# Kernel optimization log

Measured on AMD Instinct MI355X. Metric: run time of the kernel, lower is better.

## Reference

```python
import jax, jax.numpy as jnp
import numpy as np

N_MOL, E_MOL = 50000, 200000
N_PRO, E_PRO = 100000, 800000


def segment_softmax(e, seg, n):
    # e: [E, H] logits, softmax over edges grouped by target node `seg`
    m = jax.ops.segment_max(e, seg, num_segments=n)
    m = jnp.where(jnp.isfinite(m), m, jnp.zeros_like(m))
    ex = jnp.exp(e - m[seg])
    s = jax.ops.segment_sum(ex, seg, num_segments=n)
    return ex / (s[seg] + 1e-16)


def gat_conv(x, edge_index, W, a_src, a_dst, b, heads, out_ch):
    # torch_geometric GATConv (concat=True, add_self_loops=True, neg slope 0.2, eval mode)
    n = x.shape[0]
    loop = jnp.arange(n, dtype=edge_index.dtype)
    src = jnp.concatenate([edge_index[0], loop])
    dst = jnp.concatenate([edge_index[1], loop])
    h = (x @ W).reshape(n, heads, out_ch)            # [N,H,C]
    alpha_s = jnp.sum(h * a_src, axis=-1)            # [N,H]
    alpha_d = jnp.sum(h * a_dst, axis=-1)            # [N,H]
    e = jax.nn.leaky_relu(alpha_s[src] + alpha_d[dst], 0.2)  # [E,H]
    alpha = segment_softmax(e, dst, n)               # [E,H]
    out = jax.ops.segment_sum(alpha[:, :, None] * h[src], dst, num_segments=n)  # [N,H,C]
    return out.reshape(n, heads * out_ch) + b


def gcn_conv(x, edge_index, edge_weight, W, b):
    # torch_geometric GCNConv with edge_weight (add_self_loops=True, sym norm)
    n = x.shape[0]
    loop = jnp.arange(n, dtype=edge_index.dtype)
    src = jnp.concatenate([edge_index[0], loop])
    dst = jnp.concatenate([edge_index[1], loop])
    w = jnp.concatenate([edge_weight, jnp.ones((n,), x.dtype)])
    deg = jax.ops.segment_sum(w, dst, num_segments=n)
    dinv = jnp.where(deg > 0, deg ** -0.5, jnp.zeros_like(deg))
    norm = dinv[src] * w * dinv[dst]                 # [E]
    h = x @ W                                        # [N,C]
    return jax.ops.segment_sum(norm[:, None] * h[src], dst, num_segments=n) + b


def setup_inputs() -> dict:
    key = jax.random.key(0)
    ks = iter(jax.random.split(key, 32))
    rn = lambda shape, s=0.1: jax.random.normal(next(ks), shape, dtype=jnp.float32) * s
    inp = {
        "mol_x": rn((N_MOL, 78), 1.0),
        "mol_edge_index": jax.random.randint(next(ks), (2, E_MOL), 0, N_MOL, dtype=jnp.int32),
        "pro_x": rn((N_PRO, 33), 1.0),
        "pro_edge_index": jax.random.randint(next(ks), (2, E_PRO), 0, N_PRO, dtype=jnp.int32),
        "pro_edge_weight": jax.random.uniform(next(ks), (E_PRO,), dtype=jnp.float32),
        # mol_conv1: GAT 78->78, heads=2
        "W1": rn((78, 156)), "a_src1": rn((2, 78)), "a_dst1": rn((2, 78)), "b1": jnp.zeros((156,), jnp.float32),
        # mol_conv2: GAT 156->156, heads=2
        "W2": rn((156, 312)), "a_src2": rn((2, 156)), "a_dst2": rn((2, 156)), "b2": jnp.zeros((312,), jnp.float32),
        # mol_conv3: GAT 312->312, heads=1
        "W3": rn((312, 312)), "a_src3": rn((1, 312)), "a_dst3": rn((1, 312)), "b3": jnp.zeros((312,), jnp.float32),
        # pro_conv1: GCN 33->33
        "Wp1": rn((33, 33)), "bp1": jnp.zeros((33,), jnp.float32),
        # pro_conv2: GAT 33->66, heads=2
        "Wp2": rn((33, 132)), "ap_src2": rn((2, 66)), "ap_dst2": rn((2, 66)), "bp2": jnp.zeros((132,), jnp.float32),
        # pro_conv3: GAT 132->132, heads=1
        "Wp3": rn((132, 132)), "ap_src3": rn((1, 132)), "ap_dst3": rn((1, 132)), "bp3": jnp.zeros((132,), jnp.float32),
    }
    return inp


def reference(mol_x, mol_edge_index, pro_x, pro_edge_index, pro_edge_weight,
              W1, a_src1, a_dst1, b1, W2, a_src2, a_dst2, b2, W3, a_src3, a_dst3, b3,
              Wp1, bp1, Wp2, ap_src2, ap_dst2, bp2, Wp3, ap_src3, ap_dst3, bp3):
    # mol branch (per CPI_GAT.forward): conv1 -> relu -> conv2 -> relu -> conv3
    x = jax.nn.relu(gat_conv(mol_x, mol_edge_index, W1, a_src1, a_dst1, b1, 2, 78))
    x = jax.nn.relu(gat_conv(x, mol_edge_index, W2, a_src2, a_dst2, b2, 2, 156))
    x = gat_conv(x, mol_edge_index, W3, a_src3, a_dst3, b3, 1, 312)
    # pro branch: gcn -> relu -> gat -> relu -> gat -> relu
    xt = jax.nn.relu(gcn_conv(pro_x, pro_edge_index, pro_edge_weight, Wp1, bp1))
    xt = jax.nn.relu(gat_conv(xt, pro_edge_index, Wp2, ap_src2, ap_dst2, bp2, 2, 66))
    xt = jax.nn.relu(gat_conv(xt, pro_edge_index, Wp3, ap_src3, ap_dst3, bp3, 1, 132))
    return (x, xt)
```

## Files before the change

### kernel.cpp

```cpp
#include <hip/hip_runtime.h>
#include <cstdint>
#include <cstddef>

#define WAVE 64
#define NPB 4

#define TBM 128
#define TBN 128
#define TBK 32
#define LDK 40

typedef short s16x8 __attribute__((ext_vector_type(8)));
typedef float f32x4 __attribute__((ext_vector_type(4)));

__device__ __forceinline__ unsigned short f2bf(float f) {
    unsigned int u = __float_as_uint(f);
    unsigned int r = (u + 0x7fffu + ((u >> 16) & 1u)) >> 16;
    return (unsigned short)r;
}
__device__ __forceinline__ float bf2f_lo(unsigned int v) { return __uint_as_float(v << 16); }
__device__ __forceinline__ float bf2f_hi(unsigned int v) { return __uint_as_float(v & 0xffff0000u); }
__device__ __forceinline__ float lrelu02(float e) { return (e > 0.f) ? e : 0.2f * e; }


// ... 64 lines not shown
    }

#pragma unroll
    for (int mt = 0; mt < 4; mt++) {
#pragma unroll
        for (int r = 0; r < 4; r++) {
            int row = rowBase + wm + mt * 16 + quad * 4 + r;
            if (row < N) {
#pragma unroll
                for (int nt = 0; nt < 4; nt++) {
                    int col = colBase + wn + nt * 16 + l15;
                    float v = acc[mt][nt][r];
                    if (col < M) {
                        float v2 = v;
                        if (bias != nullptr) {
                            v2 += bias[col];
                            if (relu) v2 = fmaxf(v2, 0.f);
                        }
                        Cbf[(size_t)row * Mp + col] = f2bf(v2);
                    } else if (col < zpadTo) {
                        Cbf[(size_t)row * Mp + col] = 0;
                    } else if (asb != nullptr && col < M + 2 * H) {
                        int t = col - M;
                        if (t < H) asb[(size_t)row * H + t] = v;
                        else adb[(size_t)row * H + (t - H)] = v;
                    }
                }
            }
        }
    }
}


template <int SLOTS, int G, int H, bool SM, int SWEEPS, bool GCN, bool NEXTA>
__device__ __forceinline__ void agg_body(const unsigned short* __restrict__ hfeat,
                                         const float* __restrict__ as_, const float* __restrict__ ad_,
                                         const float* __restrict__ dinv,
                                         const int* __restrict__ rowp, const int2* __restrict__ cpack,
                                         const float* __restrict__ bias,
                                         float* __restrict__ out_f, unsigned short* __restrict__ out_bf,
                                         const float* __restrict__ vanf, int vald,
                                         float* __restrict__ asn, float* __restrict__ adn_o,
                                         int HC, int ldo, int relu, int n, int lane) {
    constexpr int ROWB = SWEEPS * SLOTS * 16;
    int g = lane / SLOTS;
    int slot = lane - g * SLOTS;
    bool act = (g < G);
    int C = HC / H;
    int beg = rowp[n], end = rowp[n + 1];

    float adn[H], msub[H];
    float di = 0.f;
    if (GCN) {
        di = dinv[n];
    } else {
#pragma unroll
        for (int h = 0; h < H; h++) {
            adn[h] = ad_[(size_t)n * H + h];
            msub[h] = lrelu02(as_[(size_t)n * H + h] + adn[h]);
        }
    }

    int ch0[SWEEPS];
    bool h1q[SWEEPS][4];
#pragma unroll
    for (int sw = 0; sw < SWEEPS; sw++) {
        ch0[sw] = (sw * SLOTS + slot) * 8;
#pragma unroll
        for (int q = 0; q < 4; q++) h1q[sw][q] = (H == 2) && ((ch0[sw] + 2 * q) >= C);
    }

    float sfw = GCN ? di * di : 1.f;
    float accx[SWEEPS][4], accy[SWEEPS][4];
#pragma unroll
    for (int sw = 0; sw < SWEEPS; sw++)
#pragma unroll
        for (int q = 0; q < 4; q++) { accx[sw][q] = 0.f; accy[sw][q] = 0.f; }
    if (act && g == 0) {
#pragma unroll
        for (int sw = 0; sw < SWEEPS; sw++) {
            uint4 v = *(const uint4*)((const char*)hfeat + (size_t)n * ROWB + (sw * SLOTS + slot) * 16);
            unsigned int vv[4] = {v.x, v.y, v.z, v.w};
#pragma unroll
            for (int q = 0; q < 4; q++) { accx[sw][q] = sfw * bf2f_lo(vv[q]); accy[sw][q] = sfw * bf2f_hi(vv[q]); }
        }
    }

    float wsum[H];
#pragma unroll
    for (int h = 0; h < H; h++) wsum[h] = 0.f;

    for (int base = beg; base < end; base += WAVE) {
        int cnt = end - base;
        if (cnt > WAVE) cnt = WAVE;
        int s_l = 0;
        float w_l[H];
#pragma unroll
        for (int h = 0; h < H; h++) w_l[h] = 0.f;
        if (lane < cnt) {
            int2 pk = cpack[base + lane];
            s_l = pk.x;
            if (GCN) {
                w_l[0] = dinv[s_l] * __int_as_float(pk.y) * di;
            } else {
#pragma unroll
                for (int h = 0; h < H; h++)
                    w_l[h] = __expf(lrelu02(as_[(size_t)s_l * H + h] + adn[h]) - msub[h]);
            }
            if (SM) {
#pragma unroll
                for (int h = 0; h < H; h++) wsum[h] += w_l[h];
            }
        }
        for (int j0 = 0; j0 < cnt; j0 += 2 * G) {
            int sA;
            float wA[H];
            uint4 vA[SWEEPS];
            {
                int jj = j0 + g;
                bool pad = (jj >= cnt);
                if (jj > cnt - 1) jj = cnt - 1;
                int ba = jj << 2;
                sA = __builtin_amdgcn_ds_bpermute(ba, s_l);
#pragma unroll
                for (int h = 0; h < H; h++) {
                    float t = __uint_as_float(
                        (unsigned)__builtin_amdgcn_ds_bpermute(ba, (int)__float_as_uint(w_l[h])));
                    wA[h] = pad ? 0.f : t;
                }
                if (act) {
#pragma unroll
                    for (int sw = 0; sw < SWEEPS; sw++) {
                        unsigned voff = (unsigned)sA * ROWB + (sw * SLOTS + slot) * 16;
                        vA[sw] = *(const uint4*)((const char*)hfeat + voff);
                    }
                }
            }
            bool haveB = (j0 + G < cnt);
            int sB;
            float wB[H];
            uint4 vB[SWEEPS];
            if (haveB) {
                int jj = j0 + G + g;
                bool pad = (jj >= cnt);
                if (jj > cnt - 1) jj = cnt - 1;
                int ba = jj << 2;
                sB = __builtin_amdgcn_ds_bpermute(ba, s_l);
#pragma unroll
                for (int h = 0; h < H; h++) {
                    float t = __uint_as_float(
                        (unsigned)__builtin_amdgcn_ds_bpermute(ba, (int)__float_as_uint(w_l[h])));
                    wB[h] = pad ? 0.f : t;
                }
                if (act) {
#pragma unroll
                    for (int sw = 0; sw < SWEEPS; sw++) {
                        unsigned voff = (unsigned)sB * ROWB + (sw * SLOTS + slot) * 16;
                        vB[sw] = *(const uint4*)((const char*)hfeat + voff);
                    }
                }
            }
            if (act) {
#pragma unroll
                for (int sw = 0; sw < SWEEPS; sw++) {
                    unsigned int va[4] = {vA[sw].x, vA[sw].y, vA[sw].z, vA[sw].w};
#pragma unroll
                    for (int q = 0; q < 4; q++) {
                        float wq = (H == 2) ? (h1q[sw][q] ? wA[1] : wA[0]) : wA[0];
                        accx[sw][q] += wq * bf2f_lo(va[q]);
                        accy[sw][q] += wq * bf2f_hi(va[q]);
                    }
                }
                if (haveB) {
#pragma unroll
                    for (int sw = 0; sw < SWEEPS; sw++) {
                        unsigned int ub[4] = {vB[sw].x, vB[sw].y, vB[sw].z, vB[sw].w};
#pragma unroll
                        for (int q = 0; q < 4; q++) {
                            float wq = (H == 2) ? (h1q[sw][q] ? wB[1] : wB[0]) : wB[0];
                            accx[sw][q] += wq * bf2f_lo(ub[q]);
                            accy[sw][q] += wq * bf2f_hi(ub[q]);
                        }
                    }
                }
            }
        }
    }

    if (G == 3) {
#pragma unroll
        for (int sw = 0; sw < SWEEPS; sw++)
#pragma unroll
            for (int q = 0; q < 4; q++) {
                int b1a = (lane + SLOTS) << 2, b2a = (lane + 2 * SLOTS) << 2;
                float t1 = __uint_as_float((unsigned)__builtin_amdgcn_ds_bpermute(b1a, (int)__float_as_uint(accx[sw][q])));
                float t2 = __uint_as_float((unsigned)__builtin_amdgcn_ds_bpermute(b2a, (int)__float_as_uint(accx[sw][q])));
                accx[sw][q] += t1 + t2;
                float t3 = __uint_as_float((unsigned)__builtin_amdgcn_ds_bpermute(b1a, (int)__float_as_uint(accy[sw][q])));
                float t4 = __uint_as_float((unsigned)__builtin_amdgcn_ds_bpermute(b2a, (int)__float_as_uint(accy[sw][q])));
                accy[sw][q] += t3 + t4;
            }
    } else if (G == 8) {
#pragma unroll
        for (int st = 4; st >= 1; st >>= 1) {
            int ba = (lane + st * SLOTS) << 2;
#pragma unroll
            for (int sw = 0; sw < SWEEPS; sw++)
#pragma unroll
                for (int q = 0; q < 4; q++) {
                    accx[sw][q] += __uint_as_float((unsigned)__builtin_amdgcn_ds_bpermute(ba, (int)__float_as_uint(accx[sw][q])));
                    accy[sw][q] += __uint_as_float((unsigned)__builtin_amdgcn_ds_bpermute(ba, (int)__float_as_uint(accy[sw][q])));
                }
        }
    }

    float rs[H];
    if (SM) {
#pragma unroll
        for (int h = 0; h < H; h++) {
            float t = wsum[h];
            for (int off = 32; off > 0; off >>= 1) t += __shfl_xor(t, off);
            rs[h] = 1.f / (1.f + t + 1e-16f);
        }
    } else {
#pragma unroll
        for (int h = 0; h < H; h++) rs[h] = 1.f;
    }

    float ps[4] = {0.f, 0.f, 0.f, 0.f};
    if (lane < SLOTS) {
#pragma unroll
        for (int sw = 0; sw < SWEEPS; sw++) {
            float o[8];
#pragma unroll
            for (int q = 0; q < 4; q++) {
                float r = (H == 2) ? (h1q[sw][q] ? rs[1] : rs[0]) : rs[0];
                int c0 = ch0[sw] + 2 * q;
                float b0 = (c0 < HC) ? bias[c0] : 0.f;
                float b1v = (c0 + 1 < HC) ? bias[c0 + 1] : 0.f;
                float o0 = accx[sw][q] * r + b0;
                float o1 = accy[sw][q] * r + b1v;
                if (relu) { o0 = fmaxf(o0, 0.f); o1 = fmaxf(o1, 0.f); }
                if (c0 >= HC) o0 = 0.f;
                if (c0 + 1 >= HC) o1 = 0.f;
                o[2 * q] = o0;
                o[2 * q + 1] = o1;
            }
            if (NEXTA) {
#pragma unroll
                for (int j = 0; j < 8; j++) {
                    int c = ch0[sw] + j;
#pragma unroll
                    for (int th = 0; th < 4; th++) ps[th] += o[j] * vanf[th * vald + c];
                }
            }
            if (out_bf) {
                uint4 pk;
                unsigned* pp = (unsigned*)&pk;
#pragma unroll
                for (int q = 0; q < 4; q++)
                    pp[q] = (unsigned)f2bf(o[2 * q]) | ((unsigned)f2bf(o[2 * q + 1]) << 16);
                *(uint4*)((char*)out_bf + (size_t)n * ((size_t)ldo * 2) + (sw * SLOTS + slot) * 16) = pk;
            } else {
#pragma unroll
                for (int half = 0; half < 2; half++) {
                    int c0 = ch0[sw] + half * 4;
                    if (c0 < HC) {
                        float4 f4 = make_float4(o[half * 4], o[half * 4 + 1], o[half * 4 + 2], o[half * 4 + 3]);
                        *(float4*)(out_f + (size_t)n * HC + c0) = f4;
                    }
                }
            }
        }
    }
    if (NEXTA) {
#pragma unroll
        for (int th = 0; th < 4; th++)
            for (int off = 32; off > 0; off >>= 1) ps[th] += __shfl_xor(ps[th], off);
        if (lane == 0) {
            asn[(size_t)n * 2 + 0] = ps[0];
            asn[(size_t)n * 2 + 1] = ps[1];
            adn_o[(size_t)n * 2 + 0] = ps[2];
            adn_o[(size_t)n * 2 + 1] = ps[3];
        }
    }
}


template <int SLOTS, int G>
__device__ __forceinline__ void aggN_body(const unsigned short* __restrict__ x,
                                          const float* __restrict__ as_, const float* __restrict__ ad_,
                                          const int* __restrict__ rowp, const int2* __restrict__ cpack,
                                          unsigned short* __restrict__ A2, int n, int lane) {
    constexpr int ROWB = SLOTS * 16;
    int g = lane / SLOTS;
    int slot = lane - g * SLOTS;
    bool act = (g < G);
    int beg = rowp[n], end = rowp[n + 1];

    float adn[2], msub[2];
#pragma unroll
    for (int h = 0; h < 2; h++) {
        adn[h] = ad_[(size_t)n * 2 + h];
        msub[h] = lrelu02(as_[(size_t)n * 2 + h] + adn[h]);
    }

    float ax[2][4], ay[2][4];
#pragma unroll
    for (int h = 0; h < 2; h++)
#pragma unroll
        for (int q = 0; q < 4; q++) { ax[h][q] = 0.f; ay[h][q] = 0.f; }
    if (act && g == 0) {
        uint4 v = *(const uint4*)((const char*)x + (size_t)n * ROWB + slot * 16);
        unsigned int vv[4] = {v.x, v.y, v.z, v.w};
#pragma unroll
        for (int q = 0; q < 4; q++) {
            float lo = bf2f_lo(vv[q]), hi = bf2f_hi(vv[q]);
            ax[0][q] = lo; ax[1][q] = lo;
            ay[0][q] = hi; ay[1][q] = hi;
        }
    }

    float wsum[2] = {0.f, 0.f};

    for (int base = beg; base < end; base += WAVE) {
        int cnt = end - base;
        if (cnt > WAVE) cnt = WAVE;
        int s_l = 0;
        float w_l[2] = {0.f, 0.f};
        if (lane < cnt) {
            s_l = cpack[base + lane].x;
#pragma unroll
            for (int h = 0; h < 2; h++)
                w_l[h] = __expf(lrelu02(as_[(size_t)s_l * 2 + h] + adn[h]) - msub[h]);
            wsum[0] += w_l[0];
            wsum[1] += w_l[1];
        }
        for (int j0 = 0; j0 < cnt; j0 += 2 * G) {
            int sA;
            float wA[2];
            uint4 vA;
            {
                int jj = j0 + g;
                bool pad = (jj >= cnt);
                if (jj > cnt - 1) jj = cnt - 1;
                int ba = jj << 2;
                sA = __builtin_amdgcn_ds_bpermute(ba, s_l);
#pragma unroll
                for (int h = 0; h < 2; h++) {
                    float t = __uint_as_float(
                        (unsigned)__builtin_amdgcn_ds_bpermute(ba, (int)__float_as_uint(w_l[h])));
                    wA[h] = pad ? 0.f : t;
                }
                if (act) vA = *(const uint4*)((const char*)x + (unsigned)sA * ROWB + slot * 16);
            }
            bool haveB = (j0 + G < cnt);
            int sB;
            float wB[2];
            uint4 vB;
            if (haveB) {
                int jj = j0 + G + g;
                bool pad = (jj >= cnt);
                if (jj > cnt - 1) jj = cnt - 1;
                int ba = jj << 2;
                sB = __builtin_amdgcn_ds_bpermute(ba, s_l);
#pragma unroll
                for (int h = 0; h < 2; h++) {
                    float t = __uint_as_float(
                        (unsigned)__builtin_amdgcn_ds_bpermute(ba, (int)__float_as_uint(w_l[h])));
                    wB[h] = pad ? 0.f : t;
                }
                if (act) vB = *(const uint4*)((const char*)x + (unsigned)sB * ROWB + slot * 16);
            }
            if (act) {
                unsigned int va[4] = {vA.x, vA.y, vA.z, vA.w};
#pragma unroll
                for (int q = 0; q < 4; q++) {
                    float lo = bf2f_lo(va[q]), hi = bf2f_hi(va[q]);
                    ax[0][q] += wA[0] * lo; ax[1][q] += wA[1] * lo;
                    ay[0][q] += wA[0] * hi; ay[1][q] += wA[1] * hi;
                }
                if (haveB) {
                    unsigned int ub[4] = {vB.x, vB.y, vB.z, vB.w};
#pragma unroll
                    for (int q = 0; q < 4; q++) {
                        float lo = bf2f_lo(ub[q]), hi = bf2f_hi(ub[q]);
                        ax[0][q] += wB[0] * lo; ax[1][q] += wB[1] * lo;
                        ay[0][q] += wB[0] * hi; ay[1][q] += wB[1] * hi;
                    }
                }
            }
        }
    }

    if (G == 3) {
#pragma unroll
        for (int h = 0; h < 2; h++)
#pragma unroll
            for (int q = 0; q < 4; q++) {
                int b1a = (lane + SLOTS) << 2, b2a = (lane + 2 * SLOTS) << 2;
                float t1 = __uint_as_float((unsigned)__builtin_amdgcn_ds_bpermute(b1a, (int)__float_as_uint(ax[h][q])));
                float t2 = __uint_as_float((unsigned)__builtin_amdgcn_ds_bpermute(b2a, (int)__float_as_uint(ax[h][q])));
                ax[h][q] += t1 + t2;
                float t3 = __uint_as_float((unsigned)__builtin_amdgcn_ds_bpermute(b1a, (int)__float_as_uint(ay[h][q])));
                float t4 = __uint_as_float((unsigned)__builtin_amdgcn_ds_bpermute(b2a, (int)__float_as_uint(ay[h][q])));
                ay[h][q] += t3 + t4;
            }
    } else if (G == 8) {
#pragma unroll
        for (int st = 4; st >= 1; st >>= 1) {
            int ba = (lane + st * SLOTS) << 2;
#pragma unroll
            for (int h = 0; h < 2; h++)
#pragma unroll
                for (int q = 0; q < 4; q++) {
                    ax[h][q] += __uint_as_float((unsigned)__builtin_amdgcn_ds_bpermute(ba, (int)__float_as_uint(ax[h][q])));
                    ay[h][q] += __uint_as_float((unsigned)__builtin_amdgcn_ds_bpermute(ba, (int)__float_as_uint(ay[h][q])));
                }
        }
    }

    float rs[2];
#pragma unroll
    for (int h = 0; h < 2; h++) {
        float t = wsum[h];
        for (int off = 32; off > 0; off >>= 1) t += __shfl_xor(t, off);
        rs[h] = 1.f / (1.f + t + 1e-16f);
    }

    if (lane < SLOTS) {
#pragma unroll
        for (int h = 0; h < 2; h++) {
            uint4 pk;
            unsigned* pp = (unsigned*)&pk;
#pragma unroll
            for (int q = 0; q < 4; q++) {
                float o0 = ax[h][q] * rs[h];
                float o1 = ay[h][q] * rs[h];
                pp[q] = (unsigned)f2bf(o0) | ((unsigned)f2bf(o1) << 16);
            }
            *(uint4*)((char*)A2 + (size_t)n * (2 * ROWB) + h * ROWB + slot * 16) = pk;
        }
    }
}


__device__ __forceinline__ void cvtw1(const float* __restrict__ W, unsigned short* __restrict__ WT,
                                      int K, int M, int Kp, int i) {
    int m = i / Kp;
    int k = i - m * Kp;
    WT[i] = (k < K) ? f2bf(W[(long long)k * M + m]) : (unsigned short)0;
}

__device__ __forceinline__ void cvtw_bd(const float* __restrict__ W, unsigned short* __restrict__ WT,
                                        int K, int M, int C, int Kp, int Kph, int i) {
    int m = i / Kp;
    int k = i - m * Kp;
    unsigned short v = 0;
    if (m < M) {
        int hm = m / C;
        int kk = k - hm * Kph;
        if (kk >= 0 && kk < K) v = f2bf(W[(long long)kk * M + m]);
    }
    WT[i] = v;
}

__device__ __forceinline__ void prep1(const float* __restrict__ W, const float* __restrict__ a_src,
                                      const float* __restrict__ a_dst, unsigned short* __restrict__ WT,
                                      int K, int M, int C, int Kp, int H, int b, int lane) {
    int k = b % Kp;
    int th = b / Kp;
    int t = th / H;
    int h = th - t * H;
    size_t orow = (size_t)(M + t * H + h) * Kp;
    if (k >= K) {
// ... 185 lines not shown
        int bb = b - nbs;
        gemm_body(A1, B1, C1, as1o, ad1o, bias1, relu1, zpad1, N1, Kp1, M1, Mext1, Mp1, H1, bb % g1x, bb / g1x);
    } else {
        int bb = b - nbs - nb1;
        gemm_body(A2, B2, C2, as2o, ad2o, bias2, relu2, zpad2, N2, Kp2, M2, Mext2, Mp2, H2, bb % g2x, bb / g2x);
    }
}


__global__ __launch_bounds__(256) void k_deg(const int* __restrict__ rowp, const int2* __restrict__ cpack,
                                             float* __restrict__ dinv, int N) {
    int n = blockIdx.x * 256 + threadIdx.x;
    if (n < N) {
        int b = rowp[n], e = rowp[n + 1];
        float s = 0.f;
        for (int p = b; p < e; p++) s += __int_as_float(cpack[p].y);
        dinv[n] = rsqrtf(s + 1.0f);
    }
}


__global__ __launch_bounds__(NPB * 64) void k_fuse1(
    const unsigned short* __restrict__ hb, const float* __restrict__ asm_, const float* __restrict__ adm_,
    const int* __restrict__ mrowp, const int2* __restrict__ mcp, const float* __restrict__ b1,
    unsigned short* __restrict__ x2m, const float* __restrict__ va2f,
    float* __restrict__ asm2, float* __restrict__ adm2, int Nm,
    const unsigned short* __restrict__ hbp, const float* __restrict__ dinv,
    const int* __restrict__ prowp, const int2* __restrict__ pcp, const float* __restrict__ bp1,
    unsigned short* __restrict__ x2p, const float* __restrict__ vap2f,
    float* __restrict__ asp2, float* __restrict__ adp2, int Np, int nb1) {
    int wave = threadIdx.x >> 6, lane = threadIdx.x & 63;
    int b = blockIdx.x;
    if (b < nb1) {
        int n = b * NPB + wave;
        if (n < Nm)
            agg_body<20, 3, 2, true, 1, false, true>(hb, asm_, adm_, nullptr, mrowp, mcp, b1,
                                                     nullptr, x2m, va2f, 160, asm2, adm2,
                                                     156, 160, 1, n, lane);
    } else {
        int n = (b - nb1) * NPB + wave;
        if (n < Np)
            agg_body<5, 8, 1, false, 1, true, true>(hbp, nullptr, nullptr, dinv, prowp, pcp, bp1,
                                                    nullptr, x2p, vap2f, 40, asp2, adp2,
                                                    33, 40, 1, n, lane);
    }
}

__global__ __launch_bounds__(NPB * 64) void k_fuseN(
    const unsigned short* __restrict__ x2m, const float* __restrict__ asm2, const float* __restrict__ adm2,
    const int* __restrict__ mrowp, const int2* __restrict__ mcp, unsigned short* __restrict__ xa2m, int Nm,
    const unsigned short* __restrict__ x2p, const float* __restrict__ asp2, const float* __restrict__ adp2,
    const int* __restrict__ prowp, const int2* __restrict__ pcp, unsigned short* __restrict__ xa2p, int Np,
    int nb1) {
    int wave = threadIdx.x >> 6, lane = threadIdx.x & 63;
    int b = blockIdx.x;
    if (b < nb1) {
        int n = b * NPB + wave;
        if (n < Nm) aggN_body<20, 3>(x2m, asm2, adm2, mrowp, mcp, xa2m, n, lane);
    } else {
        int n = (b - nb1) * NPB + wave;
        if (n < Np) aggN_body<5, 8>(x2p, asp2, adp2, prowp, pcp, xa2p, n, lane);
    }
}

__global__ __launch_bounds__(NPB * 64) void k_fuse5(
    const unsigned short* __restrict__ hb, const float* __restrict__ asm_, const float* __restrict__ adm_,
    const int* __restrict__ mrowp, const int2* __restrict__ mcp, const float* __restrict__ b3,
    float* __restrict__ out_mol, int Nm,
    const unsigned short* __restrict__ hbp, const float* __restrict__ asp_, const float* __restrict__ adp_,
    const int* __restrict__ prowp, const int2* __restrict__ pcp, const float* __restrict__ bp3,
    float* __restrict__ out_pro, int Np, int nb1) {
    int wave = threadIdx.x >> 6, lane = threadIdx.x & 63;
    int b = blockIdx.x;
    if (b < nb1) {
        int n = b * NPB + wave;
        if (n < Nm)
            agg_body<20, 3, 1, true, 2, false, false>(hb, asm_, adm_, nullptr, mrowp, mcp, b3,
                                                      out_mol, nullptr, nullptr, 0, nullptr, nullptr,
                                                      312, 320, 0, n, lane);
    } else {
        int n = (b - nb1) * NPB + wave;
        if (n < Np)
            agg_body<17, 3, 1, true, 1, false, false>(hbp, asp_, adp_, nullptr, prowp, pcp, bp3,
                                                      out_pro, nullptr, nullptr, 0, nullptr, nullptr,
                                                      132, 136, 1, n, lane);
    }
}


extern "C" void kernel_launch(void* const* d_in, const int* in_sizes, int n_in,
                              void* d_out, int out_size, void* d_ws, size_t ws_size,
                              hipStream_t stream) {
    const int N_MOL = in_sizes[0] / 78;
    const int E_MOL = in_sizes[1] / 2;
    const int N_PRO = in_sizes[2] / 33;
    const int E_PRO = in_sizes[3] / 2;
    const int NT = N_MOL + N_PRO;
    const int ET = E_MOL + E_PRO;

    const float* mol_x = (const float*)d_in[0];
    const int* mol_ei = (const int*)d_in[1];
    const float* pro_x = (const float*)d_in[2];
    const int* pro_ei = (const int*)d_in[3];
    const float* pro_ew = (const float*)d_in[4];
    const float *W1 = (const float*)d_in[5], *as1 = (const float*)d_in[6], *ad1 = (const float*)d_in[7],
                *b1 = (const float*)d_in[8];
    const float *W2 = (const float*)d_in[9], *as2 = (const float*)d_in[10], *ad2 = (const float*)d_in[11],
                *b2 = (const float*)d_in[12];
    const float *W3 = (const float*)d_in[13], *as3 = (const float*)d_in[14], *ad3 = (const float*)d_in[15],
                *b3 = (const float*)d_in[16];
    const float *Wp1 = (const float*)d_in[17], *bp1 = (const float*)d_in[18];
    const float *Wp2 = (const float*)d_in[19], *aps2 = (const float*)d_in[20], *apd2 = (const float*)d_in[21],
                *bp2 = (const float*)d_in[22];
    const float *Wp3 = (const float*)d_in[23], *aps3 = (const float*)d_in[24], *apd3 = (const float*)d_in[25],
                *bp3 = (const float*)d_in[26];

    float* out_mol = (float*)d_out;
    float* out_pro = (float*)d_out + (size_t)N_MOL * 312;
// ... 66 lines not shown

    hipMemsetAsync(cnt_all, 0, (size_t)NT * 4, stream);
    int nbCnt = (ET + 1023) / 1024;
    int nbCvx = (int)((totM + totP + 1023) / 1024);
    int gridA = nbCnt + 957 + 508 + nbCvx;
    k_A<<<gridA, 256, 0, stream>>>(mol_dst, pro_dst, cnt_all, N_MOL, E_MOL, ET, nbCnt,
                                   W1, W2, W3, Wp1, Wp2, Wp3, wt1, wt2bd, wt3, wtp1, wtp2bd, wtp3,
                                   as1, ad1, as2, ad2, as3, ad3, aps2, apd2, aps3, apd3,
                                   va2f, vap2f, mol_x, xb0, pro_x, xp0, totM, totP);

    int nbT = (NT + 255) / 256;
    k_scan1<<<nbT, 256, 0, stream>>>(cnt_all, incl, bsums, NT);
    k_scan2<<<1, 1024, 0, stream>>>(bsums, nbT);
    k_scan3_all<<<nbT, 256, 0, stream>>>(incl, cnt_all, bsums, mol_rowp, pro_rowp, cur_all,
                                         N_MOL, N_PRO, E_MOL, E_PRO);

    int gyM = (N_MOL + TBM - 1) / TBM;
    int gyP = (N_PRO + TBM - 1) / TBM;

    {
        int nbs = (ET + 255) / 256;
        int g1x = 2;
        int nb1 = g1x * gyM;
        int g2x = 1;
        k_B<<<nbs + nb1 + g2x * gyP, 256, 0, stream>>>(
            mol_src, mol_dst, pro_src, pro_dst, pro_ew, cur_all, cpack, N_MOL, E_MOL, ET, nbs,
            xb0, wt1, hb1, asb_m, adb_m, nullptr, 0, 0, N_MOL, 80, 156, 160, 160, 2, g1x, nb1,
            xp0, wtp1, hbp1, nullptr, nullptr, nullptr, 0, 0, N_PRO, 40, 33, 33, 40, 0, g2x);
    }

    k_deg<<<(N_PRO + 255) / 256, 256, 0, stream>>>(pro_rowp, pro_cp, dinv, N_PRO);

    {
        int nb1 = (N_MOL + NPB - 1) / NPB;
        int nb2 = (N_PRO + NPB - 1) / NPB;
        k_fuse1<<<nb1 + nb2, NPB * 64, 0, stream>>>(hb1, asb_m, adb_m, mol_rowp, mol_cp, b1,
                                                    x2m, va2f, asb_m2, adb_m2, N_MOL,
                                                    hbp1, dinv, pro_rowp, pro_cp, bp1,
                                                    x2p, vap2f, asb_p2, adb_p2, N_PRO, nb1);
    }

    {
        int nb1 = (N_MOL + NPB - 1) / NPB;
        int nb2 = (N_PRO + NPB - 1) / NPB;
        k_fuseN<<<nb1 + nb2, NPB * 64, 0, stream>>>(x2m, asb_m2, adb_m2, mol_rowp, mol_cp, xa2m, N_MOL,
                                                    x2p, asb_p2, adb_p2, pro_rowp, pro_cp, xa2p, N_PRO, nb1);
    }

    {
        int g1x = 3;
        int nb1 = g1x * gyM;
        int g2x = 2;
        k_B<<<nb1 + g2x * gyP, 256, 0, stream>>>(
            nullptr, nullptr, nullptr, nullptr, nullptr, nullptr, nullptr, N_MOL, E_MOL, ET, 0,
            xa2m, wt2bd, x3m, nullptr, nullptr, b2, 1, 320, N_MOL, 320, 312, 320, 320, 0, g1x, nb1,
            xa2p, wtp2bd, xpp, nullptr, nullptr, bp2, 1, 136, N_PRO, 80, 132, 136, 136, 0, g2x);
    }

    {
        int g1x = 3;
        int nb1 = g1x * gyM;
        int g2x = 2;
        k_B<<<nb1 + g2x * gyP, 256, 0, stream>>>(
            nullptr, nullptr, nullptr, nullptr, nullptr, nullptr, nullptr, N_MOL, E_MOL, ET, 0,
            x3m, wt3, hb3, asb_m, adb_m, nullptr, 0, 0, N_MOL, 320, 312, 314, 320, 1, g1x, nb1,
            xpp, wtp3, hbp3, asb_p, adb_p, nullptr, 0, 0, N_PRO, 136, 132, 134, 136, 1, g2x);
    }

    {
        int nb1 = (N_MOL + NPB - 1) / NPB;
        int nb2 = (N_PRO + NPB - 1) / NPB;
        k_fuse5<<<nb1 + nb2, NPB * 64, 0, stream>>>(hb3, asb_m, adb_m, mol_rowp, mol_cp, b3, out_mol, N_MOL,
                                                    hbp3, asb_p, adb_p, pro_rowp, pro_cp, bp3, out_pro, N_PRO, nb1);
    }
}
```

Measured before the change: 842.6 us.

## Map each lane group to its own node in aggregation kernels

The aggregation kernels previously assigned one node per wave and split its edge list across lane groups, using ds_bpermute to broadcast source ids and weights and cross-group reductions at the end. Now each group of SLOTS lanes handles a separate node and walks that node's edges serially, two at a time. This removes the broadcasts and the cross-group and softmax-sum reductions and cuts the block count, so more of each wave does useful work. In exchange, per-node latency becomes serial in degree, and load imbalance between nodes sharing a wave can leave lanes idle.

```diff
diff --git a/kernel.cpp b/kernel.cpp
--- a/kernel.cpp
+++ b/kernel.cpp
@@ -120,33 +120,36 @@
 }
 
 
-template <int SLOTS, int G, int H, bool SM, int SWEEPS, bool GCN, bool NEXTA>
-__device__ __forceinline__ void agg_body(const unsigned short* __restrict__ hfeat,
-                                         const float* __restrict__ as_, const float* __restrict__ ad_,
-                                         const float* __restrict__ dinv,
-                                         const int* __restrict__ rowp, const int2* __restrict__ cpack,
-                                         const float* __restrict__ bias,
-                                         float* __restrict__ out_f, unsigned short* __restrict__ out_bf,
-                                         const float* __restrict__ vanf, int vald,
-                                         float* __restrict__ asn, float* __restrict__ adn_o,
-                                         int HC, int ldo, int relu, int n, int lane) {
+template <int SLOTS, int NG, int H, bool SM, int SWEEPS, bool GCN, bool NEXTA>
+__device__ __forceinline__ void agg_gp(const unsigned short* __restrict__ hfeat,
+                                       const float* __restrict__ as_, const float* __restrict__ ad_,
+                                       const float* __restrict__ dinv,
+                                       const int* __restrict__ rowp, const int2* __restrict__ cpack,
+                                       const float* __restrict__ bias,
+                                       float* __restrict__ out_f, unsigned short* __restrict__ out_bf,
+                                       const float* __restrict__ vanf, int vald,
+                                       float* __restrict__ asn, float* __restrict__ adn_o,
+                                       int HC, int ldo, int relu, int nbase, int lane, int N) {
     constexpr int ROWB = SWEEPS * SLOTS * 16;
     int g = lane / SLOTS;
     int slot = lane - g * SLOTS;
-    bool act = (g < G);
+    int n = nbase + g;
+    if (g >= NG || n >= N) return;
     int C = HC / H;
     int beg = rowp[n], end = rowp[n + 1];
 
     float adn[H], msub[H];
-    float di = 0.f;
+    float di = 0.f, sfw;
     if (GCN) {
         di = dinv[n];
+        sfw = di * di;
     } else {
 #pragma unroll
         for (int h = 0; h < H; h++) {
             adn[h] = ad_[(size_t)n * H + h];
             msub[h] = lrelu02(as_[(size_t)n * H + h] + adn[h]);
         }
+        sfw = 1.f;
     }
 
     int ch0[SWEEPS];
@@ -158,214 +161,161 @@
         for (int q = 0; q < 4; q++) h1q[sw][q] = (H == 2) && ((ch0[sw] + 2 * q) >= C);
     }
 
-    float sfw = GCN ? di * di : 1.f;
     float accx[SWEEPS][4], accy[SWEEPS][4];
 #pragma unroll
-    for (int sw = 0; sw < SWEEPS; sw++)
-#pragma unroll
-        for (int q = 0; q < 4; q++) { accx[sw][q] = 0.f; accy[sw][q] = 0.f; }
-    if (act && g == 0) {
+    for (int sw = 0; sw < SWEEPS; sw++) {
+        uint4 v = *(const uint4*)((const char*)hfeat + (size_t)n * ROWB + (sw * SLOTS + slot) * 16);
+        unsigned int vv[4] = {v.x, v.y, v.z, v.w};
+#pragma unroll
+        for (int q = 0; q < 4; q++) { accx[sw][q] = sfw * bf2f_lo(vv[q]); accy[sw][q] = sfw * bf2f_hi(vv[q]); }
+    }
+
+    float wsum[H];
+#pragma unroll
+    for (int h = 0; h < H; h++) wsum[h] = 0.f;
+
+    int p = beg;
+    for (; p + 1 < end; p += 2) {
+        int2 pk0 = cpack[p];
+        int2 pk1 = cpack[p + 1];
+        int s0 = pk0.x, s1 = pk1.x;
+        float w0[H], w1[H];
+        if (GCN) {
+            w0[0] = dinv[s0] * __int_as_float(pk0.y) * di;
+            w1[0] = dinv[s1] * __int_as_float(pk1.y) * di;
+        } else {
+#pragma unroll
+            for (int h = 0; h < H; h++) {
+                w0[h] = __expf(lrelu02(as_[(size_t)s0 * H + h] + adn[h]) - msub[h]);
+                w1[h] = __expf(lrelu02(as_[(size_t)s1 * H + h] + adn[h]) - msub[h]);
+            }
+        }
+        if (SM) {
+#pragma unroll
+            for (int h = 0; h < H; h++) wsum[h] += w0[h] + w1[h];
+        }
+        uint4 v0[SWEEPS], v1[SWEEPS];
+#pragma unroll
+        for (int sw = 0; sw < SWEEPS; sw++)
+            v0[sw] = *(const uint4*)((const char*)hfeat + (size_t)s0 * ROWB + (sw * SLOTS + slot) * 16);
+#pragma unroll
+        for (int sw = 0; sw < SWEEPS; sw++)
+            v1[sw] = *(const uint4*)((const char*)hfeat + (size_t)s1 * ROWB + (sw * SLOTS + slot) * 16);
 #pragma unroll
         for (int sw = 0; sw < SWEEPS; sw++) {
-            uint4 v = *(const uint4*)((const char*)hfeat + (size_t)n * ROWB + (sw * SLOTS + slot) * 16);
-            unsigned int vv[4] = {v.x, v.y, v.z, v.w};
-#pragma unroll
-            for (int q = 0; q < 4; q++) { accx[sw][q] = sfw * bf2f_lo(vv[q]); accy[sw][q] = sfw * bf2f_hi(vv[q]); }
-        }
-    }
-
-    float wsum[H];
-#pragma unroll
-    for (int h = 0; h < H; h++) wsum[h] = 0.f;
-
-    for (int base = beg; base < end; base += WAVE) {
-        int cnt = end - base;
-        if (cnt > WAVE) cnt = WAVE;
-        int s_l = 0;
-        float w_l[H];
-#pragma unroll
-        for (int h = 0; h < H; h++) w_l[h] = 0.f;
-        if (lane < cnt) {
-            int2 pk = cpack[base + lane];
-            s_l = pk.x;
-            if (GCN) {
-                w_l[0] = dinv[s_l] * __int_as_float(pk.y) * di;
-            } else {
-#pragma unroll
-                for (int h = 0; h < H; h++)
-                    w_l[h] = __expf(lrelu02(as_[(size_t)s_l * H + h] + adn[h]) - msub[h]);
-            }
-            if (SM) {
-#pragma unroll
-                for (int h = 0; h < H; h++) wsum[h] += w_l[h];
-            }
-        }
-        for (int j0 = 0; j0 < cnt; j0 += 2 * G) {
-            int sA;
-            float wA[H];
-            uint4 vA[SWEEPS];
-            {
-                int jj = j0 + g;
-                bool pad = (jj >= cnt);
-                if (jj > cnt - 1) jj = cnt - 1;
-                int ba = jj << 2;
-                sA = __builtin_amdgcn_ds_bpermute(ba, s_l);
-#pragma unroll
-                for (int h = 0; h < H; h++) {
-                    float t = __uint_as_float(
-                        (unsigned)__builtin_amdgcn_ds_bpermute(ba, (int)__float_as_uint(w_l[h])));
-                    wA[h] = pad ? 0.f : t;
-                }
-                if (act) {
-#pragma unroll
-                    for (int sw = 0; sw < SWEEPS; sw++) {
-                        unsigned voff = (unsigned)sA * ROWB + (sw * SLOTS + slot) * 16;
-                        vA[sw] = *(const uint4*)((const char*)hfeat + voff);
-                    }
-                }
-            }
-            bool haveB = (j0 + G < cnt);
-            int sB;
-            float wB[H];
-            uint4 vB[SWEEPS];
-            if (haveB) {
-                int jj = j0 + G + g;
-                bool pad = (jj >= cnt);
-                if (jj > cnt - 1) jj = cnt - 1;
-                int ba = jj << 2;
-                sB = __builtin_amdgcn_ds_bpermute(ba, s_l);
-#pragma unroll
-                for (int h = 0; h < H; h++) {
-                    float t = __uint_as_float(
-                        (unsigned)__builtin_amdgcn_ds_bpermute(ba, (int)__float_as_uint(w_l[h])));
-                    wB[h] = pad ? 0.f : t;
-                }
-                if (act) {
-#pragma unroll
-                    for (int sw = 0; sw < SWEEPS; sw++) {
-                        unsigned voff = (unsigned)sB * ROWB + (sw * SLOTS + slot) * 16;
-                        vB[sw] = *(const uint4*)((const char*)hfeat + voff);
-                    }
-                }
-            }
-            if (act) {
-#pragma unroll
-                for (int sw = 0; sw < SWEEPS; sw++) {
-                    unsigned int va[4] = {vA[sw].x, vA[sw].y, vA[sw].z, vA[sw].w};
-#pragma unroll
-                    for (int q = 0; q < 4; q++) {
-                        float wq = (H == 2) ? (h1q[sw][q] ? wA[1] : wA[0]) : wA[0];
-                        accx[sw][q] += wq * bf2f_lo(va[q]);
-                        accy[sw][q] += wq * bf2f_hi(va[q]);
-                    }
-                }
-                if (haveB) {
-#pragma unroll
-                    for (int sw = 0; sw < SWEEPS; sw++) {
-                        unsigned int ub[4] = {vB[sw].x, vB[sw].y, vB[sw].z, vB[sw].w};
-#pragma unroll
-                        for (int q = 0; q < 4; q++) {
-                            float wq = (H == 2) ? (h1q[sw][q] ? wB[1] : wB[0]) : wB[0];
-                            accx[sw][q] += wq * bf2f_lo(ub[q]);
-                            accy[sw][q] += wq * bf2f_hi(ub[q]);
-                        }
-                    }
-                }
-            }
-        }
-    }
-
-    if (G == 3) {
+            unsigned int a0[4] = {v0[sw].x, v0[sw].y, v0[sw].z, v0[sw].w};
+            unsigned int a1[4] = {v1[sw].x, v1[sw].y, v1[sw].z, v1[sw].w};
+#pragma unroll
+            for (int q = 0; q < 4; q++) {
+                float wq0 = (H == 2) ? (h1q[sw][q] ? w0[1] : w0[0]) : w0[0];
+                float wq1 = (H == 2) ? (h1q[sw][q] ? w1[1] : w1[0]) : w1[0];
+                accx[sw][q] += wq0 * bf2f_lo(a0[q]) + wq1 * bf2f_lo(a1[q]);
+                accy[sw][q] += wq0 * bf2f_hi(a0[q]) + wq1 * bf2f_hi(a1[q]);
+            }
+        }
+    }
+    if (p < end) {
+        int2 pk0 = cpack[p];
+        int s0 = pk0.x;
+        float w0[H];
+        if (GCN) {
+            w0[0] = dinv[s0] * __int_as_float(pk0.y) * di;
+        } else {
+#pragma unroll
+            for (int h = 0; h < H; h++)
+                w0[h] = __expf(lrelu02(as_[(size_t)s0 * H + h] + adn[h]) - msub[h]);
+        }
+        if (SM) {
+#pragma unroll
+            for (int h = 0; h < H; h++) wsum[h] += w0[h];
+        }
+        uint4 v0[SWEEPS];
 #pragma unroll
         for (int sw = 0; sw < SWEEPS; sw++)
+            v0[sw] = *(const uint4*)((const char*)hfeat + (size_t)s0 * ROWB + (sw * SLOTS + slot) * 16);
+#pragma unroll
+        for (int sw = 0; sw < SWEEPS; sw++) {
+            unsigned int a0[4] = {v0[sw].x, v0[sw].y, v0[sw].z, v0[sw].w};
 #pragma unroll
             for (int q = 0; q < 4; q++) {
-                int b1a = (lane + SLOTS) << 2, b2a = (lane + 2 * SLOTS) << 2;
-                float t1 = __uint_as_float((unsigned)__builtin_amdgcn_ds_bpermute(b1a, (int)__float_as_uint(accx[sw][q])));
-                float t2 = __uint_as_float((unsigned)__builtin_amdgcn_ds_bpermute(b2a, (int)__float_as_uint(accx[sw][q])));
-                accx[sw][q] += t1 + t2;
-                float t3 = __uint_as_float((unsigned)__builtin_amdgcn_ds_bpermute(b1a, (int)__float_as_uint(accy[sw][q])));
-                float t4 = __uint_as_float((unsigned)__builtin_amdgcn_ds_bpermute(b2a, (int)__float_as_uint(accy[sw][q])));
-                accy[sw][q] += t3 + t4;
-            }
-    } else if (G == 8) {
-#pragma unroll
-        for (int st = 4; st >= 1; st >>= 1) {
-            int ba = (lane + st * SLOTS) << 2;
-#pragma unroll
-            for (int sw = 0; sw < SWEEPS; sw++)
-#pragma unroll
-                for (int q = 0; q < 4; q++) {
-                    accx[sw][q] += __uint_as_float((unsigned)__builtin_amdgcn_ds_bpermute(ba, (int)__float_as_uint(accx[sw][q])));
-                    accy[sw][q] += __uint_as_float((unsigned)__builtin_amdgcn_ds_bpermute(ba, (int)__float_as_uint(accy[sw][q])));
-                }
+                float wq0 = (H == 2) ? (h1q[sw][q] ? w0[1] : w0[0]) : w0[0];
+                accx[sw][q] += wq0 * bf2f_lo(a0[q]);
+                accy[sw][q] += wq0 * bf2f_hi(a0[q]);
+            }
         }
     }
 
     float rs[H];
     if (SM) {
 #pragma unroll
-        for (int h = 0; h < H; h++) {
-            float t = wsum[h];
-            for (int off = 32; off > 0; off >>= 1) t += __shfl_xor(t, off);
-            rs[h] = 1.f / (1.f + t + 1e-16f);
-        }
+        for (int h = 0; h < H; h++) rs[h] = 1.f / (1.f + wsum[h] + 1e-16f);
     } else {
 #pragma unroll
         for (int h = 0; h < H; h++) rs[h] = 1.f;
     }
 
     float ps[4] = {0.f, 0.f, 0.f, 0.f};
-    if (lane < SLOTS) {
-#pragma unroll
-        for (int sw = 0; sw < SWEEPS; sw++) {
-            float o[8];
-#pragma unroll
-            for (int q = 0; q < 4; q++) {
-                float r = (H == 2) ? (h1q[sw][q] ? rs[1] : rs[0]) : rs[0];
-                int c0 = ch0[sw] + 2 * q;
-                float b0 = (c0 < HC) ? bias[c0] : 0.f;
-                float b1v = (c0 + 1 < HC) ? bias[c0 + 1] : 0.f;
-                float o0 = accx[sw][q] * r + b0;
-                float o1 = accy[sw][q] * r + b1v;
-                if (relu) { o0 = fmaxf(o0, 0.f); o1 = fmaxf(o1, 0.f); }
-                if (c0 >= HC) o0 = 0.f;
-                if (c0 + 1 >= HC) o1 = 0.f;
-                o[2 * q] = o0;
-                o[2 * q + 1] = o1;
-            }
-            if (NEXTA) {
-#pragma unroll
-                for (int j = 0; j < 8; j++) {
-                    int c = ch0[sw] + j;
-#pragma unroll
-                    for (int th = 0; th < 4; th++) ps[th] += o[j] * vanf[th * vald + c];
+#pragma unroll
+    for (int sw = 0; sw < SWEEPS; sw++) {
+        float o[8];
+#pragma unroll
+        for (int q = 0; q < 4; q++) {
+            float r = (H == 2) ? (h1q[sw][q] ? rs[1] : rs[0]) : rs[0];
+            int c0 = ch0[sw] + 2 * q;
+            float b0 = (c0 < HC) ? bias[c0] : 0.f;
+            float b1v = (c0 + 1 < HC) ? bias[c0 + 1] : 0.f;
+            float o0 = accx[sw][q] * r + b0;
+            float o1 = accy[sw][q] * r + b1v;
+            if (relu) { o0 = fmaxf(o0, 0.f); o1 = fmaxf(o1, 0.f); }
+            if (c0 >= HC) o0 = 0.f;
+            if (c0 + 1 >= HC) o1 = 0.f;
+            o[2 * q] = o0;
+            o[2 * q + 1] = o1;
+        }
+        if (NEXTA) {
+#pragma unroll
+            for (int j = 0; j < 8; j++) {
+                int c = ch0[sw] + j;
+#pragma unroll
+                for (int th = 0; th < 4; th++) ps[th] += o[j] * vanf[th * vald + c];
+            }
+        }
+        if (out_bf) {
+            uint4 pk;
+            unsigned* pp = (unsigned*)&pk;
+#pragma unroll
+            for (int q = 0; q < 4; q++)
+                pp[q] = (unsigned)f2bf(o[2 * q]) | ((unsigned)f2bf(o[2 * q + 1]) << 16);
+            *(uint4*)((char*)out_bf + (size_t)n * ((size_t)ldo * 2) + (sw * SLOTS + slot) * 16) = pk;
+        } else {
+#pragma unroll
+            for (int half = 0; half < 2; half++) {
+                int c0 = ch0[sw] + half * 4;
+                if (c0 < HC) {
+                    float4 f4 = make_float4(o[half * 4], o[half * 4 + 1], o[half * 4 + 2], o[half * 4 + 3]);
+                    *(float4*)(out_f + (size_t)n * HC + c0) = f4;
                 }
             }
-            if (out_bf) {
-                uint4 pk;
-                unsigned* pp = (unsigned*)&pk;
-#pragma unroll
-                for (int q = 0; q < 4; q++)
-                    pp[q] = (unsigned)f2bf(o[2 * q]) | ((unsigned)f2bf(o[2 * q + 1]) << 16);
-                *(uint4*)((char*)out_bf + (size_t)n * ((size_t)ldo * 2) + (sw * SLOTS + slot) * 16) = pk;
-            } else {
-#pragma unroll
-                for (int half = 0; half < 2; half++) {
-                    int c0 = ch0[sw] + half * 4;
-                    if (c0 < HC) {
-                        float4 f4 = make_float4(o[half * 4], o[half * 4 + 1], o[half * 4 + 2], o[half * 4 + 3]);
-                        *(float4*)(out_f + (size_t)n * HC + c0) = f4;
-                    }
-                }
-            }
         }
     }
     if (NEXTA) {
-#pragma unroll
-        for (int th = 0; th < 4; th++)
-            for (int off = 32; off > 0; off >>= 1) ps[th] += __shfl_xor(ps[th], off);
-        if (lane == 0) {
+        constexpr int P = SLOTS >= 32 ? 32 : SLOTS >= 16 ? 16 : SLOTS >= 8 ? 8 : SLOTS >= 4 ? 4 : SLOTS >= 2 ? 2 : 1;
+        if (P < SLOTS) {
+#pragma unroll
+            for (int th = 0; th < 4; th++) {
+                float t = __shfl_down(ps[th], P);
+                if (slot + P < SLOTS) ps[th] += t;
+            }
+        }
+#pragma unroll
+        for (int off = P >> 1; off > 0; off >>= 1) {
+#pragma unroll
+            for (int th = 0; th < 4; th++) {
+                float t = __shfl_down(ps[th], off);
+                if (slot + off < P) ps[th] += t;
+            }
+        }
+        if (slot == 0) {
             asn[(size_t)n * 2 + 0] = ps[0];
             asn[(size_t)n * 2 + 1] = ps[1];
             adn_o[(size_t)n * 2 + 0] = ps[2];
@@ -375,15 +325,16 @@
 }
 
 
-template <int SLOTS, int G>
-__device__ __forceinline__ void aggN_body(const unsigned short* __restrict__ x,
-                                          const float* __restrict__ as_, const float* __restrict__ ad_,
-                                          const int* __restrict__ rowp, const int2* __restrict__ cpack,
-                                          unsigned short* __restrict__ A2, int n, int lane) {
+template <int SLOTS, int NG>
+__device__ __forceinline__ void aggN_gp(const unsigned short* __restrict__ x,
+                                        const float* __restrict__ as_, const float* __restrict__ ad_,
+                                        const int* __restrict__ rowp, const int2* __restrict__ cpack,
+                                        unsigned short* __restrict__ A2, int nbase, int lane, int N) {
     constexpr int ROWB = SLOTS * 16;
     int g = lane / SLOTS;
     int slot = lane - g * SLOTS;
-    bool act = (g < G);
+    int n = nbase + g;
+    if (g >= NG || n >= N) return;
     int beg = rowp[n], end = rowp[n + 1];
 
     float adn[2], msub[2];
@@ -394,11 +345,7 @@
     }
 
     float ax[2][4], ay[2][4];
-#pragma unroll
-    for (int h = 0; h < 2; h++)
-#pragma unroll
-        for (int q = 0; q < 4; q++) { ax[h][q] = 0.f; ay[h][q] = 0.f; }
-    if (act && g == 0) {
+    {
         uint4 v = *(const uint4*)((const char*)x + (size_t)n * ROWB + slot * 16);
         unsigned int vv[4] = {v.x, v.y, v.z, v.w};
 #pragma unroll
@@ -408,127 +355,69 @@
             ay[0][q] = hi; ay[1][q] = hi;
         }
     }
-
     float wsum[2] = {0.f, 0.f};
 
-    for (int base = beg; base < end; base += WAVE) {
-        int cnt = end - base;
-        if (cnt > WAVE) cnt = WAVE;
-        int s_l = 0;
-        float w_l[2] = {0.f, 0.f};
-        if (lane < cnt) {
-            s_l = cpack[base + lane].x;
-#pragma unroll
-            for (int h = 0; h < 2; h++)
-                w_l[h] = __expf(lrelu02(as_[(size_t)s_l * 2 + h] + adn[h]) - msub[h]);
-            wsum[0] += w_l[0];
-            wsum[1] += w_l[1];
-        }
-        for (int j0 = 0; j0 < cnt; j0 += 2 * G) {
-            int sA;
-            float wA[2];
-            uint4 vA;
-            {
-                int jj = j0 + g;
-                bool pad = (jj >= cnt);
-                if (jj > cnt - 1) jj = cnt - 1;
-                int ba = jj << 2;
-                sA = __builtin_amdgcn_ds_bpermute(ba, s_l);
-#pragma unroll
-                for (int h = 0; h < 2; h++) {
-                    float t = __uint_as_float(
-                        (unsigned)__builtin_amdgcn_ds_bpermute(ba, (int)__float_as_uint(w_l[h])));
-                    wA[h] = pad ? 0.f : t;
-                }
-                if (act) vA = *(const uint4*)((const char*)x + (unsigned)sA * ROWB + slot * 16);
-            }
-            bool haveB = (j0 + G < cnt);
-            int sB;
-            float wB[2];
-            uint4 vB;
-            if (haveB) {
-                int jj = j0 + G + g;
-                bool pad = (jj >= cnt);
-                if (jj > cnt - 1) jj = cnt - 1;
-                int ba = jj << 2;
-                sB = __builtin_amdgcn_ds_bpermute(ba, s_l);
-#pragma unroll
-                for (int h = 0; h < 2; h++) {
-                    float t = __uint_as_float(
-                        (unsigned)__builtin_amdgcn_ds_bpermute(ba, (int)__float_as_uint(w_l[h])));
-                    wB[h] = pad ? 0.f : t;
-                }
-                if (act) vB = *(const uint4*)((const char*)x + (unsigned)sB * ROWB + slot * 16);
-            }
-            if (act) {
-                unsigned int va[4] = {vA.x, vA.y, vA.z, vA.w};
-#pragma unroll
-                for (int q = 0; q < 4; q++) {
-                    float lo = bf2f_lo(va[q]), hi = bf2f_hi(va[q]);
-                    ax[0][q] += wA[0] * lo; ax[1][q] += wA[1] * lo;
-                    ay[0][q] += wA[0] * hi; ay[1][q] += wA[1] * hi;
-                }
-                if (haveB) {
-                    unsigned int ub[4] = {vB.x, vB.y, vB.z, vB.w};
-#pragma unroll
-                    for (int q = 0; q < 4; q++) {
-                        float lo = bf2f_lo(ub[q]), hi = bf2f_hi(ub[q]);
-                        ax[0][q] += wB[0] * lo; ax[1][q] += wB[1] * lo;
-                        ay[0][q] += wB[0] * hi; ay[1][q] += wB[1] * hi;
-                    }
-                }
-            }
-        }
-    }
-
-    if (G == 3) {
+    int p = beg;
+    for (; p + 1 < end; p += 2) {
+        int s0 = cpack[p].x;
+        int s1 = cpack[p + 1].x;
+        float w0[2], w1[2];
+#pragma unroll
+        for (int h = 0; h < 2; h++) {
+            w0[h] = __expf(lrelu02(as_[(size_t)s0 * 2 + h] + adn[h]) - msub[h]);
+            w1[h] = __expf(lrelu02(as_[(size_t)s1 * 2 + h] + adn[h]) - msub[h]);
+        }
+        wsum[0] += w0[0] + w1[0];
+        wsum[1] += w0[1] + w1[1];
+        uint4 v0 = *(const uint4*)((const char*)x + (size_t)s0 * ROWB + slot * 16);
+        uint4 v1 = *(const uint4*)((const char*)x + (size_t)s1 * ROWB + slot * 16);
+        unsigned int a0[4] = {v0.x, v0.y, v0.z, v0.w};
+        unsigned int a1[4] = {v1.x, v1.y, v1.z, v1.w};
+#pragma unroll
+        for (int q = 0; q < 4; q++) {
+            float lo0 = bf2f_lo(a0[q]), hi0 = bf2f_hi(a0[q]);
+            float lo1 = bf2f_lo(a1[q]), hi1 = bf2f_hi(a1[q]);
+            ax[0][q] += w0[0] * lo0 + w1[0] * lo1;
+            ax[1][q] += w0[1] * lo0 + w1[1] * lo1;
+            ay[0][q] += w0[0] * hi0 + w1[0] * hi1;
+            ay[1][q] += w0[1] * hi0 + w1[1] * hi1;
+        }
+    }
+    if (p < end) {
+        int s0 = cpack[p].x;
+        float w0[2];
 #pragma unroll
         for (int h = 0; h < 2; h++)
-#pragma unroll
-            for (int q = 0; q < 4; q++) {
-                int b1a = (lane + SLOTS) << 2, b2a = (lane + 2 * SLOTS) << 2;
-                float t1 = __uint_as_float((unsigned)__builtin_amdgcn_ds_bpermute(b1a, (int)__float_as_uint(ax[h][q])));
-                float t2 = __uint_as_float((unsigned)__builtin_amdgcn_ds_bpermute(b2a, (int)__float_as_uint(ax[h][q])));
-                ax[h][q] += t1 + t2;
-                float t3 = __uint_as_float((unsigned)__builtin_amdgcn_ds_bpermute(b1a, (int)__float_as_uint(ay[h][q])));
-                float t4 = __uint_as_float((unsigned)__builtin_amdgcn_ds_bpermute(b2a, (int)__float_as_uint(ay[h][q])));
-                ay[h][q] += t3 + t4;
-            }
-    } else if (G == 8) {
-#pragma unroll
-        for (int st = 4; st >= 1; st >>= 1) {
-            int ba = (lane + st * SLOTS) << 2;
-#pragma unroll
-            for (int h = 0; h < 2; h++)
-#pragma unroll
-                for (int q = 0; q < 4; q++) {
-                    ax[h][q] += __uint_as_float((unsigned)__builtin_amdgcn_ds_bpermute(ba, (int)__float_as_uint(ax[h][q])));
-                    ay[h][q] += __uint_as_float((unsigned)__builtin_amdgcn_ds_bpermute(ba, (int)__float_as_uint(ay[h][q])));
-                }
+            w0[h] = __expf(lrelu02(as_[(size_t)s0 * 2 + h] + adn[h]) - msub[h]);
+        wsum[0] += w0[0];
+        wsum[1] += w0[1];
+        uint4 v0 = *(const uint4*)((const char*)x + (size_t)s0 * ROWB + slot * 16);
+        unsigned int a0[4] = {v0.x, v0.y, v0.z, v0.w};
+#pragma unroll
+        for (int q = 0; q < 4; q++) {
+            float lo0 = bf2f_lo(a0[q]), hi0 = bf2f_hi(a0[q]);
+            ax[0][q] += w0[0] * lo0;
+            ax[1][q] += w0[1] * lo0;
+            ay[0][q] += w0[0] * hi0;
+            ay[1][q] += w0[1] * hi0;
         }
     }
 
     float rs[2];
 #pragma unroll
+    for (int h = 0; h < 2; h++) rs[h] = 1.f / (1.f + wsum[h] + 1e-16f);
+
+#pragma unroll
     for (int h = 0; h < 2; h++) {
-        float t = wsum[h];
-        for (int off = 32; off > 0; off >>= 1) t += __shfl_xor(t, off);
-        rs[h] = 1.f / (1.f + t + 1e-16f);
-    }
-
-    if (lane < SLOTS) {
-#pragma unroll
-        for (int h = 0; h < 2; h++) {
-            uint4 pk;
-            unsigned* pp = (unsigned*)&pk;
-#pragma unroll
-            for (int q = 0; q < 4; q++) {
-                float o0 = ax[h][q] * rs[h];
-                float o1 = ay[h][q] * rs[h];
-                pp[q] = (unsigned)f2bf(o0) | ((unsigned)f2bf(o1) << 16);
-            }
-            *(uint4*)((char*)A2 + (size_t)n * (2 * ROWB) + h * ROWB + slot * 16) = pk;
-        }
+        uint4 pk;
+        unsigned* pp = (unsigned*)&pk;
+#pragma unroll
+        for (int q = 0; q < 4; q++) {
+            float o0 = ax[h][q] * rs[h];
+            float o1 = ay[h][q] * rs[h];
+            pp[q] = (unsigned)f2bf(o0) | ((unsigned)f2bf(o1) << 16);
+        }
+        *(uint4*)((char*)A2 + (size_t)n * (2 * ROWB) + h * ROWB + slot * 16) = pk;
     }
 }
 
@@ -780,17 +669,15 @@
     int wave = threadIdx.x >> 6, lane = threadIdx.x & 63;
     int b = blockIdx.x;
     if (b < nb1) {
-        int n = b * NPB + wave;
-        if (n < Nm)
-            agg_body<20, 3, 2, true, 1, false, true>(hb, asm_, adm_, nullptr, mrowp, mcp, b1,
-                                                     nullptr, x2m, va2f, 160, asm2, adm2,
-                                                     156, 160, 1, n, lane);
+        int nbase = (b * NPB + wave) * 3;
+        agg_gp<20, 3, 2, true, 1, false, true>(hb, asm_, adm_, nullptr, mrowp, mcp, b1,
+                                               nullptr, x2m, va2f, 160, asm2, adm2,
+                                               156, 160, 1, nbase, lane, Nm);
     } else {
-        int n = (b - nb1) * NPB + wave;
-        if (n < Np)
-            agg_body<5, 8, 1, false, 1, true, true>(hbp, nullptr, nullptr, dinv, prowp, pcp, bp1,
-                                                    nullptr, x2p, vap2f, 40, asp2, adp2,
-                                                    33, 40, 1, n, lane);
+        int nbase = ((b - nb1) * NPB + wave) * 12;
+        agg_gp<5, 12, 1, false, 1, true, true>(hbp, nullptr, nullptr, dinv, prowp, pcp, bp1,
+                                               nullptr, x2p, vap2f, 40, asp2, adp2,
+                                               33, 40, 1, nbase, lane, Np);
     }
 }
 
@@ -803,11 +690,11 @@
     int wave = threadIdx.x >> 6, lane = threadIdx.x & 63;
     int b = blockIdx.x;
     if (b < nb1) {
-        int n = b * NPB + wave;
-        if (n < Nm) aggN_body<20, 3>(x2m, asm2, adm2, mrowp, mcp, xa2m, n, lane);
+        int nbase = (b * NPB + wave) * 3;
+        aggN_gp<20, 3>(x2m, asm2, adm2, mrowp, mcp, xa2m, nbase, lane, Nm);
     } else {
-        int n = (b - nb1) * NPB + wave;
-        if (n < Np) aggN_body<5, 8>(x2p, asp2, adp2, prowp, pcp, xa2p, n, lane);
+        int nbase = ((b - nb1) * NPB + wave) * 12;
+        aggN_gp<5, 12>(x2p, asp2, adp2, prowp, pcp, xa2p, nbase, lane, Np);
     }
 }
 
@@ -821,17 +708,15 @@
     int wave = threadIdx.x >> 6, lane = threadIdx.x & 63;
     int b = blockIdx.x;
     if (b < nb1) {
-        int n = b * NPB + wave;
-        if (n < Nm)
-            agg_body<20, 3, 1, true, 2, false, false>(hb, asm_, adm_, nullptr, mrowp, mcp, b3,
-                                                      out_mol, nullptr, nullptr, 0, nullptr, nullptr,
-                                                      312, 320, 0, n, lane);
+        int nbase = (b * NPB + wave) * 3;
+        agg_gp<20, 3, 1, true, 2, false, false>(hb, asm_, adm_, nullptr, mrowp, mcp, b3,
+                                                out_mol, nullptr, nullptr, 0, nullptr, nullptr,
+                                                312, 320, 0, nbase, lane, Nm);
     } else {
-        int n = (b - nb1) * NPB + wave;
-        if (n < Np)
-            agg_body<17, 3, 1, true, 1, false, false>(hbp, asp_, adp_, nullptr, prowp, pcp, bp3,
-                                                      out_pro, nullptr, nullptr, 0, nullptr, nullptr,
-                                                      132, 136, 1, n, lane);
+        int nbase = ((b - nb1) * NPB + wave) * 3;
+        agg_gp<17, 3, 1, true, 1, false, false>(hbp, asp_, adp_, nullptr, prowp, pcp, bp3,
+                                                out_pro, nullptr, nullptr, 0, nullptr, nullptr,
+                                                132, 136, 1, nbase, lane, Np);
     }
 }
 
@@ -964,8 +849,8 @@
     k_deg<<<(N_PRO + 255) / 256, 256, 0, stream>>>(pro_rowp, pro_cp, dinv, N_PRO);
 
     {
-        int nb1 = (N_MOL + NPB - 1) / NPB;
-        int nb2 = (N_PRO + NPB - 1) / NPB;
+        int nb1 = (N_MOL + NPB * 3 - 1) / (NPB * 3);
+        int nb2 = (N_PRO + NPB * 12 - 1) / (NPB * 12);
         k_fuse1<<<nb1 + nb2, NPB * 64, 0, stream>>>(hb1, asb_m, adb_m, mol_rowp, mol_cp, b1,
                                                     x2m, va2f, asb_m2, adb_m2, N_MOL,
                                                     hbp1, dinv, pro_rowp, pro_cp, bp1,
@@ -973,8 +858,8 @@
     }
 
     {
-        int nb1 = (N_MOL + NPB - 1) / NPB;
-        int nb2 = (N_PRO + NPB - 1) / NPB;
+        int nb1 = (N_MOL + NPB * 3 - 1) / (NPB * 3);
+        int nb2 = (N_PRO + NPB * 12 - 1) / (NPB * 12);
         k_fuseN<<<nb1 + nb2, NPB * 64, 0, stream>>>(x2m, asb_m2, adb_m2, mol_rowp, mol_cp, xa2m, N_MOL,
                                                     x2p, asb_p2, adb_p2, pro_rowp, pro_cp, xa2p, N_PRO, nb1);
     }
@@ -1000,8 +885,8 @@
     }
 
     {
-        int nb1 = (N_MOL + NPB - 1) / NPB;
-        int nb2 = (N_PRO + NPB - 1) / NPB;
+        int nb1 = (N_MOL + NPB * 3 - 1) / (NPB * 3);
+        int nb2 = (N_PRO + NPB * 3 - 1) / (NPB * 3);
         k_fuse5<<<nb1 + nb2, NPB * 64, 0, stream>>>(hb3, asb_m, adb_m, mol_rowp, mol_cp, b3, out_mol, N_MOL,
                                                     hbp3, asb_p, adb_p, pro_rowp, pro_cp, bp3, out_pro, N_PRO, nb1);
     }
```

After: 707.1 us. -16.1%, faster.
